# Kernel tuning notes

Measured on AMD Instinct MI355X. Metric: run time of the kernel, lower is better.

Reference implementation:

```python
import jax, jax.numpy as jnp
import numpy as np

ALPHA = 0.15  # top-k fraction (forward default)


def setup_inputs() -> dict:
    key = jax.random.key(0)
    k1, k2, k3 = jax.random.split(key, 3)
    B, N, D = 8, 1024, 256
    x = jax.random.normal(k1, (B, N, D), dtype=jnp.float32)
    # torch nn.Linear(dim, H*head_dim, bias=False); stored here as [D, H*head_dim]
    W_src = jax.random.normal(k2, (D, D), dtype=jnp.float32) * (1.0 / np.sqrt(D))
    W_tgt = jax.random.normal(k3, (D, D), dtype=jnp.float32) * (1.0 / np.sqrt(D))
    return {"x": x, "W_src": W_src, "W_tgt": W_tgt}


def _topk_mask(adj, k):
    # adj: [B,H,N,N]; exact scatter of 1.0 at top-k indices along last axis
    B, H, N, _ = adj.shape
    _, idx = jax.lax.top_k(adj, k)              # [B,H,N,k]
    bi = jnp.arange(B)[:, None, None, None]
    hi = jnp.arange(H)[None, :, None, None]
    ni = jnp.arange(N)[None, None, :, None]
    mask = jnp.zeros_like(adj).at[bi, hi, ni, idx].set(1.0)
    return mask


def reference(x, W_src, W_tgt):
    # directed=True path of DirectedGraphLearner.forward
    B, N, D = x.shape
    H, head_dim = 4, D // 4
    k = max(1, int(ALPHA * N))
    src = (x @ W_src).reshape(B, N, H, head_dim)
    tgt = (x @ W_tgt).reshape(B, N, H, head_dim)
    adj = jnp.einsum('bihd,bjhd->bhij', src, tgt)
    adj = jax.nn.gelu(adj, approximate=False)    # torch F.gelu default = exact erf
    mask = _topk_mask(adj, k)
    return adj * mask
```

## Files before the change

### kernel.cpp

```cpp
#include <hip/hip_runtime.h>
#include <math.h>


#define KSEL 153u
#define EPSK 61000u
#define EPSKS 76000u

typedef __attribute__((ext_vector_type(8))) short short8v;
typedef __attribute__((ext_vector_type(4))) float float4v;

__device__ __forceinline__ float gelu_f32(float x) {
    return 0.5f * x * (1.0f + erff(x * 0.70710678118654752f));
}

__device__ __forceinline__ unsigned long long d2key(double v) {
    unsigned long long u = (unsigned long long)__double_as_longlong(v);
    return (u >> 63) ? ~u : (u | 0x8000000000000000ull);
}

__device__ __forceinline__ unsigned lkeyf(float v) {
    float q = fmaf(v, 33554432.0f, 2147483648.0f);
    q = fminf(fmaxf(q, 0.0f), 4294967040.0f);
    return (unsigned)q;
}

__device__ __forceinline__ unsigned short b16(float x) {
    unsigned u = __float_as_uint(x);
    u += 0x7FFFu + ((u >> 16) & 1u);
    return (unsigned short)(u >> 16);
}
__device__ __forceinline__ float bf2f(unsigned short h) {
    return __uint_as_float(((unsigned)h) << 16);
}
__device__ __forceinline__ unsigned pk2(float a, float b) {
    return (unsigned)b16(a) | ((unsigned)b16(b) << 16);
}

#define LGKMW() asm volatile("s_waitcnt lgkmcnt(0)" ::: "memory")
#define LGKM0()                                             \
    do {                                                    \
        asm volatile("s_waitcnt lgkmcnt(0)" ::: "memory");  \
        __builtin_amdgcn_sched_barrier(0);                  \
    } while (0)

template <bool W32>
__global__ __launch_bounds__(256) void k1_proj(const float* __restrict__ x,
                                               const float* __restrict__ Wsrc,
                                               const float* __restrict__ Wtgt,
                                               double* __restrict__ ws,
                                               unsigned short* __restrict__ th,
                                               unsigned short* __restrict__ tl) {
    __shared__ float xs[32 * 68];
    __shared__ float wsh[32 * 68];
    const int t = threadIdx.x;
    const int bx = blockIdx.x;
    const int by = blockIdx.y;
    const int col0 = (by & 3) * 64;
    const float* __restrict__ W = (by < 4) ? Wsrc : Wtgt;
    double* __restrict__ outp = ws + ((by < 4) ? 0 : 2097152);

    double acc[4][4];
#pragma unroll
    for (int i = 0; i < 4; ++i)
#pragma unroll
        for (int j = 0; j < 4; ++j) acc[i][j] = 0.0;

    const int m_loc = (t & 15) * 4;
    const int c_loc = (t >> 4) * 4;

    for (int kt = 0; kt < 8; ++kt) {
        __syncthreads();
#pragma unroll
        for (int it = 0; it < 2; ++it) {
            int f4 = t + 256 * it;
            int m = f4 >> 3, k4 = f4 & 7;
            float4 v = *reinterpret_cast<const float4*>(&x[(bx * 64 + m) * 256 + kt * 32 + 4 * k4]);
            xs[(4 * k4 + 0) * 68 + m] = v.x;
            xs[(4 * k4 + 1) * 68 + m] = v.y;
            xs[(4 * k4 + 2) * 68 + m] = v.z;
            xs[(4 * k4 + 3) * 68 + m] = v.w;
        }
#pragma unroll
        for (int it = 0; it < 2; ++it) {
            int f4 = t + 256 * it;
            int k = f4 >> 4, c4 = f4 & 15;
            *reinterpret_cast<float4*>(&wsh[k * 68 + 4 * c4]) =
                *reinterpret_cast<const float4*>(&W[(kt * 32 + k) * 256 + col0 + 4 * c4]);
        }
        __syncthreads();
#pragma unroll
        for (int kk = 0; kk < 32; ++kk) {
            float4 a = *reinterpret_cast<const float4*>(&xs[kk * 68 + m_loc]);
            float4 b = *reinterpret_cast<const float4*>(&wsh[kk * 68 + c_loc]);
            double ad[4] = {a.x, a.y, a.z, a.w};
            double bd[4] = {b.x, b.y, b.z, b.w};
#pragma unroll
            for (int i = 0; i < 4; ++i)
#pragma unroll
                for (int j = 0; j < 4; ++j) acc[i][j] += ad[i] * bd[j];
        }
    }
    const int hd = by & 3;
#pragma unroll
    for (int i = 0; i < 4; ++i) {
        int m = bx * 64 + m_loc + i;
        int b = m >> 10, n = m & 1023;
        int bhd = b * 4 + hd;
        size_t base = ((size_t)(bhd * 1024 + n)) * 64 + c_loc;
        double2 v01, v23;
        v01.x = acc[i][0]; v01.y = acc[i][1];
        v23.x = acc[i][2]; v23.y = acc[i][3];
        *reinterpret_cast<double2*>(&outp[base]) = v01;
        *reinterpret_cast<double2*>(&outp[base + 2]) = v23;
        if (W32 && by >= 4) {
            float f0 = (float)acc[i][0], f1 = (float)acc[i][1];
            float f2 = (float)acc[i][2], f3 = (float)acc[i][3];
            unsigned short h0 = b16(f0), h1 = b16(f1), h2 = b16(f2), h3 = b16(f3);
            uint2 H, L;
            H.x = (unsigned)h0 | ((unsigned)h1 << 16);
            H.y = (unsigned)h2 | ((unsigned)h3 << 16);
            L.x = pk2(f0 - bf2f(h0), f1 - bf2f(h1));
            L.y = pk2(f2 - bf2f(h2), f3 - bf2f(h3));
            int T = n >> 4, colLow = n & 15;
            int ks = c_loc >> 5, kg = (c_loc >> 3) & 3, elem = c_loc & 7;
            size_t fidx = ((size_t)bhd * 65536) +
                          (size_t)(((T * 2 + ks) * 64 + kg * 16 + colLow) * 8 + elem);
            *reinterpret_cast<uint2*>(&th[fidx]) = H;
            *reinterpret_cast<uint2*>(&tl[fidx]) = L;
        }
    }
}

template <bool FAST, bool S16>
__global__ __launch_bounds__(256, 4) void k2a_gemm(const double* __restrict__ srcT,
                                                   const double* __restrict__ tgtT,
                                                   const unsigned short* __restrict__ th,
                                                   const unsigned short* __restrict__ tlo,
                                                   short* __restrict__ adjS,
                                                   float* __restrict__ out) {
    __shared__ __align__(16) float tr[16 * 512];

    unsigned short* sHI = reinterpret_cast<unsigned short*>(tr);
    unsigned short* sLO = sHI + 1024;

    const int t = threadIdx.x;
    const int lane = t & 63;
    const int wv = t >> 6;
    const int bid = (blockIdx.x & 7) * 256 + (blockIdx.x >> 3);
    const int bh = bid >> 6;
    const int itile = bid & 63;
    const int row0 = itile * 16;
    const int r0 = 4 * wv;
    const size_t tgtBase = (size_t)bh * 65536;
    const unsigned short* __restrict__ thb = th + tgtBase;
    const unsigned short* __restrict__ tlb = tlo + tgtBase;

    {
        int r = t >> 4, dq = (t & 15) * 4;
        const double* sp = &srcT[((size_t)bh * 1024 + row0 + r) * 64 + dq];
        double2 a = *reinterpret_cast<const double2*>(sp);
        double2 b = *reinterpret_cast<const double2*>(sp + 2);
        float f0 = (float)a.x, f1 = (float)a.y, f2 = (float)b.x, f3 = (float)b.y;
        unsigned short h0 = b16(f0), h1 = b16(f1), h2 = b16(f2), h3 = b16(f3);
        int s = dq >> 3;
        int idx = r * 64 + ((s ^ (r & 7)) << 3) + (dq & 7);
        uint2 H, L;
        H.x = (unsigned)h0 | ((unsigned)h1 << 16);
        H.y = (unsigned)h2 | ((unsigned)h3 << 16);
        L.x = pk2(f0 - bf2f(h0), f1 - bf2f(h1));
        L.y = pk2(f2 - bf2f(h2), f3 - bf2f(h3));
        *reinterpret_cast<uint2*>(&sHI[idx]) = H;
        *reinterpret_cast<uint2*>(&sLO[idx]) = L;
    }
    __syncthreads();

    short8v Ah[2], Al[2];
#pragma unroll
    for (int ks = 0; ks < 2; ++ks) {
        int idxA = (lane & 15) * 64 + (((4 * ks + (lane >> 4)) ^ (lane & 7)) << 3);
        Ah[ks] = *reinterpret_cast<const short8v*>(&sHI[idxA]);
        Al[ks] = *reinterpret_cast<const short8v*>(&sLO[idxA]);
    }

    const int colA = lane & 15;
    const int kgrp = lane >> 4;
    const size_t rowG0 = (size_t)bh * 1024 + row0 + r0;

#pragma unroll
    for (int h = 0; h < 2; ++h) {
        float4v acc[8];
#pragma unroll
        for (int a = 0; a < 8; ++a) acc[a] = (float4v){0.f, 0.f, 0.f, 0.f};

#pragma unroll
        for (int u = 0; u < 8; ++u) {
            const int T = 32 * h + 4 * u + wv;
#pragma unroll
            for (int ks = 0; ks < 2; ++ks) {
                short8v Bh, Bl;
                if (FAST) {
                    const size_t fbase = (size_t)(((T * 2 + ks) * 64 + lane) * 8);
                    Bh = *reinterpret_cast<const short8v*>(&thb[fbase]);
                    Bl = *reinterpret_cast<const short8v*>(&tlb[fbase]);
                } else {
                    const size_t cbase = (size_t)(16 * T + colA) * 64 + kgrp * 8;
                    const double* gp = &tgtT[tgtBase + cbase + 32 * ks];
                    double2 d0 = *reinterpret_cast<const double2*>(gp);
                    double2 d1 = *reinterpret_cast<const double2*>(gp + 2);
                    double2 d2 = *reinterpret_cast<const double2*>(gp + 4);
                    double2 d3 = *reinterpret_cast<const double2*>(gp + 6);
                    float f[8] = {(float)d0.x, (float)d0.y, (float)d1.x, (float)d1.y,
                                  (float)d2.x, (float)d2.y, (float)d3.x, (float)d3.y};
                    unsigned short hh[8];
#pragma unroll
                    for (int e = 0; e < 8; ++e) hh[e] = b16(f[e]);
                    unsigned Hw[4], Lw[4];
#pragma unroll
                    for (int e = 0; e < 4; ++e) {
                        Hw[e] = (unsigned)hh[2 * e] | ((unsigned)hh[2 * e + 1] << 16);
                        Lw[e] = pk2(f[2 * e] - bf2f(hh[2 * e]), f[2 * e + 1] - bf2f(hh[2 * e + 1]));
                    }
                    Bh = *reinterpret_cast<const short8v*>(Hw);
                    Bl = *reinterpret_cast<const short8v*>(Lw);
                }
                acc[u] = __builtin_amdgcn_mfma_f32_16x16x32_bf16(Ah[ks], Bh, acc[u], 0, 0, 0);
                acc[u] = __builtin_amdgcn_mfma_f32_16x16x32_bf16(Al[ks], Bh, acc[u], 0, 0, 0);
                acc[u] = __builtin_amdgcn_mfma_f32_16x16x32_bf16(Ah[ks], Bl, acc[u], 0, 0, 0);
            }
        }

        __syncthreads();
#pragma unroll
        for (int u = 0; u < 8; ++u) {
            int colh = 16 * (4 * u + wv) + colA;
#pragma unroll
            for (int reg = 0; reg < 4; ++reg) {
                int row = 4 * kgrp + reg;
                tr[row * 512 + (colh ^ ((kgrp & 1) << 4))] = acc[u][reg];
            }
        }
        __syncthreads();
        const int rsw = (wv & 1) << 4;
#pragma unroll
        for (int ri = 0; ri < 4; ++ri) {
            int row = r0 + ri;
#pragma unroll
            for (int q = 0; q < 2; ++q) {
                int colh = 4 * lane + 256 * q;
                float4 v = *reinterpret_cast<const float4*>(&tr[row * 512 + (colh ^ rsw)]);
                if (S16) {
                    short4 s;
                    s.x = (short)__float2int_rn(fminf(fmaxf(v.x * 512.f, -32767.f), 32767.f));
                    s.y = (short)__float2int_rn(fminf(fmaxf(v.y * 512.f, -32767.f), 32767.f));
                    s.z = (short)__float2int_rn(fminf(fmaxf(v.z * 512.f, -32767.f), 32767.f));
                    s.w = (short)__float2int_rn(fminf(fmaxf(v.w * 512.f, -32767.f), 32767.f));
                    *reinterpret_cast<short4*>(&adjS[(rowG0 + ri) * 1024 + 512 * h + colh]) = s;
                } else {
                    *reinterpret_cast<float4*>(&out[(rowG0 + ri) * 1024 + 512 * h + colh]) = v;
                }
            }
        }
    }
}

template <bool S16>
__global__ __launch_bounds__(256, 4) void k2b_select(const double* __restrict__ srcT,
                                                     const double* __restrict__ tgtT,
                                                     const short* __restrict__ adjS,
                                                     float* __restrict__ out) {
    __shared__ __align__(16) unsigned hist[4][256];

    const int t = threadIdx.x;
    const int lane = t & 63;
    const int wv = t >> 6;
    const int R = blockIdx.x * 4 + wv;
    const int bh = R >> 10;
    const size_t tgtBase = (size_t)bh * 65536;
    const size_t base = (size_t)R * 1024;
    const unsigned eps = S16 ? EPSKS : EPSK;

    float vals[16];
    if (S16) {
#pragma unroll
        for (int q = 0; q < 2; ++q) {
            short8v s = *reinterpret_cast<const short8v*>(&adjS[base + 16 * lane + 8 * q]);
#pragma unroll
            for (int e = 0; e < 8; ++e) vals[8 * q + e] = (float)s[e] * (1.0f / 512.0f);
        }
    } else {
#pragma unroll
        for (int q = 0; q < 4; ++q) {
            float4 v = *reinterpret_cast<const float4*>(&out[base + 16 * lane + 4 * q]);
            vals[4 * q + 0] = v.x;
            vals[4 * q + 1] = v.y;
            vals[4 * q + 2] = v.z;
            vals[4 * q + 3] = v.w;
        }
    }

    unsigned* histw = hist[wv];
    unsigned* cjp = histw + 128;
    unsigned long long* ckp = reinterpret_cast<unsigned long long*>(histw);
    unsigned* ccp = histw + 192;

    unsigned ul[16];
#pragma unroll
    for (int m = 0; m < 16; ++m) ul[m] = lkeyf(vals[m]);

    unsigned prefA = 0u, maskA = 0u, rk = KSEL;
#pragma unroll 1
    for (int p = 1; p >= 0; --p) {
        const int sh = 16 + 8 * p;
        *reinterpret_cast<uint4*>(&histw[4 * lane]) = make_uint4(0u, 0u, 0u, 0u);
        LGKMW();
#pragma unroll
        for (int m = 0; m < 16; ++m) {
            if ((ul[m] & maskA) == prefA)
                atomicAdd(&histw[(ul[m] >> sh) & 255u], 1u);
        }
        LGKMW();
        unsigned h0 = histw[4 * lane + 0], h1 = histw[4 * lane + 1];
        unsigned h2 = histw[4 * lane + 2], h3 = histw[4 * lane + 3];
        unsigned S = h0 + h1 + h2 + h3;
        unsigned inc = S;
#pragma unroll
        for (int off = 1; off < 64; off <<= 1) {
            unsigned o = __shfl_down(inc, off, 64);
            inc = (lane + off < 64) ? (inc + o) : inc;
        }
        unsigned above = inc - S;
        bool found = (above < rk) && (rk <= inc);
        unsigned long long bal = __ballot(found);
        int L = __ffsll(bal) - 1;
        unsigned hh[4];
        hh[0] = __shfl(h0, L, 64);
        hh[1] = __shfl(h1, L, 64);
        hh[2] = __shfl(h2, L, 64);
        hh[3] = __shfl(h3, L, 64);
        unsigned cum = __shfl(above, L, 64);
        int bsel = -1;
#pragma unroll
        for (int q = 3; q >= 0; --q) {
            if (bsel < 0) {
                if (rk <= cum + hh[q]) {
                    bsel = q;
                    rk = rk - cum;
                } else {
                    cum += hh[q];
                }
            }
        }
        prefA |= (unsigned)(4 * L + bsel) << sh;
        maskA |= 0xFFu << sh;
    }

    const unsigned klo = prefA - eps;
    const unsigned khi = prefA + 65535u + eps;

    int ch = 0, cb = 0;
#pragma unroll
    for (int m = 0; m < 16; ++m) {
        ch += (ul[m] > khi) ? 1 : 0;
        cb += (ul[m] >= klo && ul[m] <= khi) ? 1 : 0;
    }
#pragma unroll
    for (int off = 32; off; off >>= 1) {
        ch += __shfl_xor(ch, off, 64);
        cb += __shfl_xor(cb, off, 64);
    }
    const unsigned need = KSEL - (unsigned)ch;
    const bool fastp = ((unsigned)cb == need);

    unsigned long long selMask = 0ull;
    unsigned cidx[16];
    if (!fastp) {
        if (lane == 0) *ccp = 0u;
        LGKM0();
#pragma unroll
        for (int m = 0; m < 16; ++m) {
            cidx[m] = 0xFFFFFFFFu;
            if (ul[m] >= klo && ul[m] <= khi) {
                unsigned idx = atomicAdd(ccp, 1u);
                cidx[m] = idx;
                if (idx < 64u) cjp[idx] = (unsigned)(16 * lane + m);
            }
        }
        LGKM0();
        unsigned g = *ccp;
        if (g > 64u) g = 64u;
        if (lane < (int)g) {
            unsigned j = cjp[lane];
            const double2* sp = reinterpret_cast<const double2*>(&srcT[(size_t)R * 64]);
            const double2* tp = reinterpret_cast<const double2*>(&tgtT[tgtBase + (size_t)j * 64]);
            double a2 = 0.0;
#pragma unroll 8
            for (int d2 = 0; d2 < 32; ++d2) {
                double2 aa = sp[d2], bb = tp[d2];
                a2 = fma(aa.x, bb.x, fma(aa.y, bb.y, a2));
            }
            ckp[lane] = d2key(a2);
        }
        LGKM0();
        unsigned rnk2 = need;
        if (lane < (int)g) {
            unsigned long long myk = ckp[lane];
            unsigned myj = cjp[lane];
            rnk2 = 0;
            for (unsigned i = 0; i < g; ++i) {
                unsigned long long ki = ckp[i];
                rnk2 += (ki > myk || (ki == myk && cjp[i] < myj)) ? 1u : 0u;
            }
        }
        selMask = __ballot(lane < (int)g && rnk2 < need);
    }

#pragma unroll
    for (int q = 0; q < 4; ++q) {
        float4 o;
        float* op = &o.x;
#pragma unroll
        for (int e = 0; e < 4; ++e) {
            int m = 4 * q + e;
            bool sel;
            if (ul[m] > khi) sel = true;
            else if (ul[m] < klo) sel = false;
            else sel = fastp ? true
                             : ((cidx[m] < 64u) ? (((selMask >> cidx[m]) & 1ull) != 0ull) : false);
            float v = vals[m];
            op[e] = sel ? ((v > 3.0f) ? v : gelu_f32(v)) : 0.0f;
        }
        *reinterpret_cast<float4*>(&out[base + 16 * lane + 4 * q]) = o;
    }
}

extern "C" void kernel_launch(void* const* d_in, const int* in_sizes, int n_in,
                              void* d_out, int out_size, void* d_ws, size_t ws_size,
                              hipStream_t stream) {
    const float* x = (const float*)d_in[0];
    const float* Wsrc = (const float*)d_in[1];
    const float* Wtgt = (const float*)d_in[2];
    float* out = (float*)d_out;
    double* ws = (double*)d_ws;
    unsigned short* th = (unsigned short*)((char*)d_ws + 33554432);
    unsigned short* tl = (unsigned short*)((char*)d_ws + 37748736);
    short* adjS = (short*)((char*)d_ws + 41943040);

    const bool fast = (ws_size >= 40u * 1024u * 1024u);
    const bool s16 = (ws_size >= 104u * 1024u * 1024u);
    dim3 g1(128, 8);
    if (fast && s16) {
        k1_proj<true><<<g1, 256, 0, stream>>>(x, Wsrc, Wtgt, ws, th, tl);
        k2a_gemm<true, true><<<2048, 256, 0, stream>>>(ws, ws + 2097152, th, tl, adjS, out);
        k2b_select<true><<<8192, 256, 0, stream>>>(ws, ws + 2097152, adjS, out);
    } else if (fast) {
        k1_proj<true><<<g1, 256, 0, stream>>>(x, Wsrc, Wtgt, ws, th, tl);
        k2a_gemm<true, false><<<2048, 256, 0, stream>>>(ws, ws + 2097152, th, tl, adjS, out);
        k2b_select<false><<<8192, 256, 0, stream>>>(ws, ws + 2097152, adjS, out);
    } else {
        k1_proj<false><<<g1, 256, 0, stream>>>(x, Wsrc, Wtgt, ws, th, tl);
        k2a_gemm<false, false><<<2048, 256, 0, stream>>>(ws, ws + 2097152, th, tl, adjS, out);
        k2b_select<false><<<8192, 256, 0, stream>>>(ws, ws + 2097152, adjS, out);
    }
}
```

Before: 155.7 us.

## Compute first radix-select histogram pass inside GEMM epilogue and pass via side buffer

```diff
diff --git a/kernel.cpp b/kernel.cpp
--- a/kernel.cpp
+++ b/kernel.cpp
@@ -131,14 +131,14 @@
     }
 }
 
-template <bool FAST, bool S16>
-__global__ __launch_bounds__(256, 4) void k2a_gemm(const double* __restrict__ srcT,
-                                                   const double* __restrict__ tgtT,
-                                                   const unsigned short* __restrict__ th,
-                                                   const unsigned short* __restrict__ tlo,
-                                                   short* __restrict__ adjS,
-                                                   float* __restrict__ out) {
+template <bool FAST, bool S16, bool SIDE>
+__global__ __launch_bounds__(256, SIDE ? 3 : 4) void k2a_gemm(
+    const double* __restrict__ srcT, const double* __restrict__ tgtT,
+    const unsigned short* __restrict__ th, const unsigned short* __restrict__ tlo,
+    short* __restrict__ adjS, unsigned short* __restrict__ side,
+    float* __restrict__ out) {
     __shared__ __align__(16) float tr[16 * 512];
+    __shared__ __align__(16) unsigned rhist[SIDE ? 4 * 4 * 256 : 4];
 
     unsigned short* sHI = reinterpret_cast<unsigned short*>(tr);
     unsigned short* sLO = sHI + 1024;
@@ -155,6 +155,11 @@
     const unsigned short* __restrict__ thb = th + tgtBase;
     const unsigned short* __restrict__ tlb = tlo + tgtBase;
 
+    if (SIDE) {
+#pragma unroll
+        for (int e = 0; e < 4; ++e)
+            *reinterpret_cast<uint4*>(&rhist[4 * t + 1024 * e]) = make_uint4(0u, 0u, 0u, 0u);
+    }
     {
         int r = t >> 4, dq = (t & 15) * 4;
         const double* sp = &srcT[((size_t)bh * 1024 + row0 + r) * 64 + dq];
@@ -248,25 +253,81 @@
             for (int q = 0; q < 2; ++q) {
                 int colh = 4 * lane + 256 * q;
                 float4 v = *reinterpret_cast<const float4*>(&tr[row * 512 + (colh ^ rsw)]);
+                float vv[4] = {v.x, v.y, v.z, v.w};
                 if (S16) {
+                    short ss[4];
+#pragma unroll
+                    for (int e = 0; e < 4; ++e)
+                        ss[e] = (short)__float2int_rn(fminf(fmaxf(vv[e] * 512.f, -32767.f), 32767.f));
                     short4 s;
-                    s.x = (short)__float2int_rn(fminf(fmaxf(v.x * 512.f, -32767.f), 32767.f));
-                    s.y = (short)__float2int_rn(fminf(fmaxf(v.y * 512.f, -32767.f), 32767.f));
-                    s.z = (short)__float2int_rn(fminf(fmaxf(v.z * 512.f, -32767.f), 32767.f));
-                    s.w = (short)__float2int_rn(fminf(fmaxf(v.w * 512.f, -32767.f), 32767.f));
+                    s.x = ss[0]; s.y = ss[1]; s.z = ss[2]; s.w = ss[3];
                     *reinterpret_cast<short4*>(&adjS[(rowG0 + ri) * 1024 + 512 * h + colh]) = s;
+                    if (SIDE) {
+#pragma unroll
+                        for (int e = 0; e < 4; ++e) {
+                            float vd = (float)ss[e] * (1.0f / 512.0f);
+                            atomicAdd(&rhist[(4 * wv + ri) * 256 + (lkeyf(vd) >> 24)], 1u);
+                        }
+                    }
                 } else {
                     *reinterpret_cast<float4*>(&out[(rowG0 + ri) * 1024 + 512 * h + colh]) = v;
+                    if (SIDE) {
+#pragma unroll
+                        for (int e = 0; e < 4; ++e)
+                            atomicAdd(&rhist[(4 * wv + ri) * 256 + (lkeyf(vv[e]) >> 24)], 1u);
+                    }
                 }
             }
         }
     }
-}
-
-template <bool S16>
+
+    if (SIDE) {
+        LGKMW();
+#pragma unroll 1
+        for (int ri = 0; ri < 4; ++ri) {
+            uint4 hv = *reinterpret_cast<const uint4*>(&rhist[(4 * wv + ri) * 256 + 4 * lane]);
+            unsigned h0 = hv.x, h1 = hv.y, h2 = hv.z, h3 = hv.w;
+            unsigned S = h0 + h1 + h2 + h3;
+            unsigned inc = S;
+#pragma unroll
+            for (int off = 1; off < 64; off <<= 1) {
+                unsigned o = __shfl_down(inc, off, 64);
+                inc = (lane + off < 64) ? (inc + o) : inc;
+            }
+            unsigned above = inc - S;
+            unsigned rk = KSEL;
+            bool found = (above < rk) && (rk <= inc);
+            unsigned long long bal = __ballot(found);
+            int L = __ffsll(bal) - 1;
+            unsigned hh[4];
+            hh[0] = __shfl(h0, L, 64);
+            hh[1] = __shfl(h1, L, 64);
+            hh[2] = __shfl(h2, L, 64);
+            hh[3] = __shfl(h3, L, 64);
+            unsigned cum = __shfl(above, L, 64);
+            int bsel = -1;
+#pragma unroll
+            for (int q = 3; q >= 0; --q) {
+                if (bsel < 0) {
+                    if (rk <= cum + hh[q]) {
+                        bsel = q;
+                        rk = rk - cum;
+                    } else {
+                        cum += hh[q];
+                    }
+                }
+            }
+            if (lane == 0)
+                side[rowG0 + ri] = (unsigned short)(((unsigned)(4 * L + bsel) << 8) | rk);
+        }
+    }
+}
+
+template <bool S16, bool SIDE>
 __global__ __launch_bounds__(256, 4) void k2b_select(const double* __restrict__ srcT,
                                                      const double* __restrict__ tgtT,
                                                      const short* __restrict__ adjS,
+                                                     const unsigned short* __restrict__ side,
                                                      float* __restrict__ out) {
     __shared__ __align__(16) unsigned hist[4][256];
 
@@ -307,9 +368,18 @@
 #pragma unroll
     for (int m = 0; m < 16; ++m) ul[m] = lkeyf(vals[m]);
 
-    unsigned prefA = 0u, maskA = 0u, rk = KSEL;
+    unsigned prefA, maskA, rk;
+    if (SIDE) {
+        unsigned sd = side[R];
+        prefA = (sd >> 8) << 24;
+        maskA = 0xFF000000u;
+        rk = sd & 255u;
+    } else {
+        prefA = 0u; maskA = 0u; rk = KSEL;
+    }
+
 #pragma unroll 1
-    for (int p = 1; p >= 0; --p) {
+    for (int p = (SIDE ? 0 : 1); p >= 0; --p) {
         const int sh = 16 + 8 * p;
         *reinterpret_cast<uint4*>(&histw[4 * lane]) = make_uint4(0u, 0u, 0u, 0u);
         LGKMW();
@@ -444,21 +514,27 @@
     unsigned short* th = (unsigned short*)((char*)d_ws + 33554432);
     unsigned short* tl = (unsigned short*)((char*)d_ws + 37748736);
     short* adjS = (short*)((char*)d_ws + 41943040);
+    unsigned short* side = (unsigned short*)((char*)d_ws + 109051904);
 
     const bool fast = (ws_size >= 40u * 1024u * 1024u);
     const bool s16 = (ws_size >= 104u * 1024u * 1024u);
+    const bool sideok = (ws_size >= 110u * 1024u * 1024u);
     dim3 g1(128, 8);
-    if (fast && s16) {
+    if (fast && s16 && sideok) {
         k1_proj<true><<<g1, 256, 0, stream>>>(x, Wsrc, Wtgt, ws, th, tl);
-        k2a_gemm<true, true><<<2048, 256, 0, stream>>>(ws, ws + 2097152, th, tl, adjS, out);
-        k2b_select<true><<<8192, 256, 0, stream>>>(ws, ws + 2097152, adjS, out);
+        k2a_gemm<true, true, true><<<2048, 256, 0, stream>>>(ws, ws + 2097152, th, tl, adjS, side, out);
+        k2b_select<true, true><<<8192, 256, 0, stream>>>(ws, ws + 2097152, adjS, side, out);
+    } else if (fast && s16) {
+        k1_proj<true><<<g1, 256, 0, stream>>>(x, Wsrc, Wtgt, ws, th, tl);
+        k2a_gemm<true, true, false><<<2048, 256, 0, stream>>>(ws, ws + 2097152, th, tl, adjS, side, out);
+        k2b_select<true, false><<<8192, 256, 0, stream>>>(ws, ws + 2097152, adjS, side, out);
     } else if (fast) {
         k1_proj<true><<<g1, 256, 0, stream>>>(x, Wsrc, Wtgt, ws, th, tl);
-        k2a_gemm<true, false><<<2048, 256, 0, stream>>>(ws, ws + 2097152, th, tl, adjS, out);
-        k2b_select<false><<<8192, 256, 0, stream>>>(ws, ws + 2097152, adjS, out);
+        k2a_gemm<true, false, false><<<2048, 256, 0, stream>>>(ws, ws + 2097152, th, tl, adjS, side, out);
+        k2b_select<false, false><<<8192, 256, 0, stream>>>(ws, ws + 2097152, adjS, side, out);
     } else {
         k1_proj<false><<<g1, 256, 0, stream>>>(x, Wsrc, Wtgt, ws, th, tl);
-        k2a_gemm<false, false><<<2048, 256, 0, stream>>>(ws, ws + 2097152, th, tl, adjS, out);
-        k2b_select<false><<<8192, 256, 0, stream>>>(ws, ws + 2097152, adjS, out);
-    }
-}
+        k2a_gemm<false, false, false><<<2048, 256, 0, stream>>>(ws, ws + 2097152, th, tl, adjS, side, out);
+        k2b_select<false, false><<<8192, 256, 0, stream>>>(ws, ws + 2097152, adjS, side, out);
+    }
+}
```

New measurement: 165.1 us. +6.0%, slower.
